# Optimization experiments

Measured on AMD Instinct MI355X. Metric: run time of the kernel, lower is better.

The kernel has to match this reference:

```python
import jax, jax.numpy as jnp
import numpy as np

B, S1, S2, H, DW = 64, 512, 512, 768, 200


def setup_inputs() -> dict:
    key = jax.random.key(0)
    ks = jax.random.split(key, 16)
    inp = {
        'x1': jax.random.normal(ks[0], (B, S1, H), jnp.float32),
        'x1_h': jax.random.normal(ks[1], (B, H), jnp.float32),
        'x1_mask': jax.random.randint(ks[2], (B, S1), 0, 2, jnp.int32),
        'y': jax.random.normal(ks[3], (B, S1), jnp.float32),
        'x2': jax.random.normal(ks[4], (B, S2, H), jnp.float32),
        'x2_h': jax.random.normal(ks[5], (B, H), jnp.float32),
        'x2_mask': jax.random.randint(ks[6], (B, S2), 0, 2, jnp.int32),
        'tt': jax.random.normal(ks[7], (B, S1, DW), jnp.float32),
        'tt2': jax.random.normal(ks[8], (B, S2, DW), jnp.float32),
        # parameters (xavier ~ N(0, 2/(fan_in+fan_out)))
        'W_bert': jax.random.normal(ks[9], (H + 1, H), jnp.float32) * np.sqrt(2.0 / (H + 1 + H)),
        'W_wv': jax.random.normal(ks[10], (DW + 1, DW), jnp.float32) * np.sqrt(2.0 / (DW + 1 + DW)),
        'lin_wv_w': jax.random.normal(ks[11], (DW, H), jnp.float32) * np.sqrt(1.0 / DW),
        'lin_wv_b': jnp.zeros((H,), jnp.float32),
        'lin_w': jax.random.normal(ks[12], (4 * H, 1), jnp.float32) * np.sqrt(1.0 / (4 * H)),
        'lin_b': jnp.zeros((1,), jnp.float32),
    }
    return inp


def _branch(x_cat, W, keys_vals, x1_inv, x2_inv):
    # x_cat: [B,S1,D+1], W: [D+1,D], keys_vals: [B,S2,D]
    xw = jnp.matmul(x_cat, W)                                  # [B,S1,D]
    a = jnp.einsum('bsd,btd->bst', xw, keys_vals)              # [B,S1,S2]
    a = jnp.where(x2_inv[:, None, :], jnp.float32(-1e-5), a)   # faithful: tiny mask value, pre-softmax
    a = jax.nn.softmax(a, axis=-1)
    v = jnp.einsum('bst,btd->bsd', a, keys_vals)               # [B,S1,D]
    v = jnp.where(x1_inv[:, :, None], jnp.float32(-1e5), v)
    return v.max(axis=1)                                       # max-pool over S1 -> [B,D]


def reference(x1, x1_h, x1_mask, y, x2, x2_h, x2_mask, tt, tt2,
              W_bert, W_wv, lin_wv_w, lin_wv_b, lin_w, lin_b):
    x1_inv = (1 - x1_mask).astype(bool)  # True where padded
    x2_inv = (1 - x2_mask).astype(bool)

    # word-vector branch
    x1_wv = jnp.concatenate([tt, y[:, :, None]], axis=-1)      # [B,S1,201]
    x12_wv = _branch(x1_wv, W_wv, tt2, x1_inv, x2_inv)         # [B,200]
    x12_wv = x12_wv @ lin_wv_w + lin_wv_b                      # [B,768]

    # bert branch
    x1c = jnp.concatenate([x1, y[:, :, None]], axis=-1)        # [B,S1,769]
    x12 = _branch(x1c, W_bert, x2, x1_inv, x2_inv)             # [B,768]

    h = jnp.concatenate([x1_h, x2_h, x12, x12_wv], axis=1)     # [B,3072]
    o = jax.nn.sigmoid(h @ lin_w + lin_b)                      # [B,1]
    return (o, x1_inv.astype(jnp.int32), x2_inv.astype(jnp.int32))
```

## Files before the change

### kernel.cpp

```cpp
#include <hip/hip_runtime.h>


#define BB 64
#define SS 512
#define HH 768
#define DWW 200

typedef __attribute__((ext_vector_type(8))) _Float16 f16x8;
typedef __attribute__((ext_vector_type(4))) _Float16 f16x4;
typedef __attribute__((ext_vector_type(4))) float f32x4;
typedef unsigned int u32;

__device__ __forceinline__ u32 fkey(float f) {
    u32 u = __float_as_uint(f);
    return (u & 0x80000000u) ? ~u : (u | 0x80000000u);
}
__device__ __forceinline__ float fdec(u32 k) {
    u32 u = (k & 0x80000000u) ? (k & 0x7fffffffu) : ~k;
    return __uint_as_float(u);
}
__device__ __forceinline__ f32x4 mm(f16x8 a, f16x8 b, f32x4 c) {
    return __builtin_amdgcn_mfma_f32_16x16x32_f16(a, b, c, 0, 0, 0);
}
__device__ __forceinline__ void gl16(const void* g, void* l) {
    __builtin_amdgcn_global_load_lds(
        (const __attribute__((address_space(1))) void*)g,
        (__attribute__((address_space(3))) void*)l, 16, 0, 0);
}

__global__ __launch_bounds__(256) void k_setup(
    const int* __restrict__ m1, const int* __restrict__ m2,
    const float* __restrict__ Wb, const float* __restrict__ Wwv,
    float* __restrict__ out, u32* __restrict__ k1, u32* __restrict__ k2,
    int* __restrict__ idx, int* __restrict__ rcnt,
    _Float16* __restrict__ wbTH, _Float16* __restrict__ wwTH) {
    int bid = blockIdx.x, tid = threadIdx.x;
    if (bid < 128) {
        int i = bid * 256 + tid;
        out[BB + i]           = (float)(1 - m1[i]);
        out[BB + BB * SS + i] = (float)(1 - m2[i]);
    } else if (bid < 320) {
        int i = (bid - 128) * 256 + tid;
        u32 v = fkey(-1e5f);
        if (i < BB * HH) k1[i] = v;
        if (i < BB * DWW) k2[i] = v;
    } else if (bid < 384) {
        int b = bid - 320;
        if (tid < 64) {
            int base = 0;
#pragma unroll
            for (int c = 0; c < 8; ++c) {
                int s = c * 64 + tid;
                int v = m1[b * SS + s];
                unsigned long long bal = __ballot(v != 0);
                int pre = __popcll(bal & ((1ull << tid) - 1ull));
                if (v) idx[b * SS + base + pre] = s;
                base += __popcll(bal);
            }
            if (tid == 0) rcnt[b] = base;
        }
    } else if (bid < 2784) {
        int i = (bid - 384) * 256 + tid;
        int n = i / 800, k = i - n * 800;
        wbTH[i] = (_Float16)((k < 769) ? Wb[(size_t)k * 768 + n] : 0.f);
    } else {
        int i = (bid - 2784) * 256 + tid;
        int n = i / 224, k = i - n * 224;
        wwTH[i] = (_Float16)((k < 201 && n < 200) ? Wwv[(size_t)k * 200 + n] : 0.f);
    }
}

__global__ __launch_bounds__(256) void k_prep(
    const float* __restrict__ x2, const float* __restrict__ tt2,
    const float* __restrict__ x1, const float* __restrict__ tt,
    const float* __restrict__ yv,
    const int* __restrict__ idx, const int* __restrict__ rcnt,
    _Float16* __restrict__ kvB, _Float16* __restrict__ kvTB,
    _Float16* __restrict__ kvW, _Float16* __restrict__ kvTW,
    _Float16* __restrict__ XcB, _Float16* __restrict__ XcW,
    int cb, int b0) {
    __shared__ float tile[64][65];
    int bx = blockIdx.x, tid = threadIdx.x;
    if (bx < cb * 128) {
        int cbi = bx >> 7, sub = bx & 127;
        int t0 = (sub & 7) * 64, ybr = sub >> 3;
        const float* src; _Float16* kv; _Float16* kvT; int D, DPAD, DTPAD, d0;
        if (ybr < 12) { src = x2;  kv = kvB; kvT = kvTB; D = 768; DPAD = 768; DTPAD = 768; d0 = ybr * 64; }
        else          { src = tt2; kv = kvW; kvT = kvTW; D = 200; DPAD = 256; DTPAD = 256; d0 = (ybr - 12) * 64; }
        int bg = b0 + cbi;
        int tq = tid >> 3, c8 = (tid & 7) * 8;
#pragma unroll
        for (int i = 0; i < 2; ++i) {
            int t = tq + i * 32;
            int gd = d0 + c8;
            float v[8];
            if (gd + 7 < D) {
                const float* rp = src + ((size_t)bg * SS + t0 + t) * D + gd;
                float4 p0 = *(const float4*)(rp);
                float4 p1 = *(const float4*)(rp + 4);
                v[0] = p0.x; v[1] = p0.y; v[2] = p0.z; v[3] = p0.w;
                v[4] = p1.x; v[5] = p1.y; v[6] = p1.z; v[7] = p1.w;
            } else {
#pragma unroll
                for (int j = 0; j < 8; ++j) {
                    int d = gd + j;
                    v[j] = (d < D) ? src[((size_t)bg * SS + t0 + t) * D + d] : 0.f;
                }
            }
            f16x8 o;
#pragma unroll
            for (int j = 0; j < 8; ++j) {
                tile[t][c8 + j] = v[j];
                o[j] = (_Float16)v[j];
            }
            *(f16x8*)(kv + ((size_t)cbi * SS + t0 + t) * DPAD + gd) = o;
        }
        __syncthreads();
#pragma unroll
        for (int i = 0; i < 2; ++i) {
            int dl = tq + i * 32, gdr = d0 + dl;
            f16x8 o;
#pragma unroll
            for (int j = 0; j < 8; ++j) o[j] = (_Float16)tile[c8 + j][dl];
            *(f16x8*)(kvT + ((size_t)cbi * DTPAD + gdr) * SS + t0 + c8) = o;
        }
    } else {
        bx -= cb * 128;
        int cbi = bx >> 8, xb = bx & 255;
        int bg = b0 + cbi;
        const float* X; _Float16* outp; int Din, KPAD; size_t ost;
        if (xb < 200) { X = x1; outp = XcB; Din = 768; KPAD = 800; ost = (size_t)cbi * 409600; }
        else { xb -= 200; X = tt; outp = XcW; Din = 200; KPAD = 224; ost = (size_t)cbi * 114688; }
        int i8 = (xb * 256 + tid) * 8;
        int s = i8 / KPAD, k0 = i8 - s * KPAD;
        int rc = rcnt[bg];
        int rpad = (rc + 127) & ~127;
        if (s >= rpad) return;
        f16x8 o = {};
        if (s < rc) {
            int sg = idx[bg * SS + s];
            const float* Xr = X + ((size_t)bg * SS + sg) * Din;
            if (k0 + 7 < Din) {
                float4 p0 = *(const float4*)(Xr + k0);
                float4 p1 = *(const float4*)(Xr + k0 + 4);
                o[0] = (_Float16)p0.x; o[1] = (_Float16)p0.y;
                o[2] = (_Float16)p0.z; o[3] = (_Float16)p0.w;
                o[4] = (_Float16)p1.x; o[5] = (_Float16)p1.y;
                o[6] = (_Float16)p1.z; o[7] = (_Float16)p1.w;
            } else {
#pragma unroll
                for (int j = 0; j < 8; ++j) {
                    int k = k0 + j;
                    float v = (k < Din) ? Xr[k]
                                        : ((k == Din) ? yv[(size_t)bg * SS + sg] : 0.f);
                    o[j] = (_Float16)v;
                }
            }
        }
        *(f16x8*)(outp + ost + (size_t)s * KPAD + k0) = o;
    }
}

template<int KA, int KST, int TN, int SXW, int DV, int AS, int BS, int EPI>
__device__ __forceinline__ void mm_core(
    const _Float16* __restrict__ A, const _Float16* __restrict__ B,
    _Float16* __restrict__ O, const float* __restrict__ rsum,
    u32* __restrict__ keys, int jb, const int* __restrict__ rcnt,
    int b0, char* lds, float* rsv) {
    int cbi = jb / (4 * TN);
    int rest = jb - cbi * (4 * TN);
    int ts = rest / TN, tn = rest - ts * TN;
    int s0 = ts * 128, n0 = tn * 128;

    int rc = rcnt[b0 + cbi];
    int rpad = (rc + 127) & ~127;
    if (s0 >= rpad) return;

    int tid = threadIdx.x, lane = tid & 63, wid = tid >> 6;
    int wr = wid >> 1, wc = wid & 1;
    int l15 = lane & 15, sl = lane >> 4, gb = sl * 4;

    const _Float16* srcA = A + (size_t)cbi * AS + (size_t)s0 * KA;
    const _Float16* srcB = B + (size_t)cbi * BS + (size_t)n0 * KA;

    if constexpr (EPI == 2) {
        if (tid < 128) rsv[tid] = rsum[cbi * SS + s0 + tid];
    }

    f32x4 zz = {0.f, 0.f, 0.f, 0.f};
    f32x4 acc[4][4];
#pragma unroll
    for (int i = 0; i < 4; ++i)
#pragma unroll
        for (int j = 0; j < 4; ++j) acc[i][j] = zz;

#define STAGE(buf, ks)                                                        \
    _Pragma("unroll") for (int i = 0; i < 4; ++i) {                           \
        int c = wid + 4 * i;                                                  \
        int arr = c >> 3, sub = c & 7, slot = sub >> 1, rh = sub & 1;         \
        const _Float16* gp = (arr ? srcB : srcA) +                            \
            (size_t)(rh * 64 + lane) * KA + (ks) * 32 + slot * 8;             \
        gl16(gp, lds + (buf) * 16384 + c * 1024);                             \
    }

    STAGE(0, 0);
    __syncthreads();
    int buf = 0;
#pragma unroll
    for (int ks = 0; ks < KST; ++ks) {
        if (ks + 1 < KST) STAGE(buf ^ 1, ks + 1);
        char* base = lds + buf * 16384;
        f16x8 a[4], b[4];
#pragma unroll
        for (int mf = 0; mf < 4; ++mf)
            a[mf] = *(const f16x8*)(base + sl * 2048 + (wr * 64 + mf * 16 + l15) * 16);
#pragma unroll
        for (int nf = 0; nf < 4; ++nf)
            b[nf] = *(const f16x8*)(base + 8192 + sl * 2048 + (wc * 64 + nf * 16 + l15) * 16);
#pragma unroll
        for (int mf = 0; mf < 4; ++mf)
#pragma unroll
            for (int nf = 0; nf < 4; ++nf)
                acc[mf][nf] = mm(a[mf], b[nf], acc[mf][nf]);
        __syncthreads();
        buf ^= 1;
    }
#undef STAGE

    if constexpr (EPI == 1) {
        _Float16* ce = (_Float16*)lds;
#pragma unroll
        for (int mf = 0; mf < 4; ++mf)
#pragma unroll
            for (int nf = 0; nf < 4; ++nf)
#pragma unroll
                for (int r = 0; r < 4; ++r) {
                    int row = wr * 64 + mf * 16 + gb + r;
                    int col = wc * 64 + nf * 16 + l15;
                    ce[row * 128 + col] = (_Float16)acc[mf][nf][r];
                }
        __syncthreads();
#pragma unroll
        for (int i = 0; i < 8; ++i) {
            int t = tid + i * 256;
            int row = t >> 4, col = (t & 15) * 8;
            *(f16x8*)(O + ((size_t)cbi * SS + s0 + row) * SXW + n0 + col) =
                *(const f16x8*)(ce + row * 128 + col);
        }
    } else {
        int bg = b0 + cbi;
#pragma unroll
        for (int nf = 0; nf < 4; ++nf) {
            float mx = -3.0e38f;
#pragma unroll
            for (int mf = 0; mf < 4; ++mf)
#pragma unroll
                for (int r = 0; r < 4; ++r) {
                    int srow = wr * 64 + mf * 16 + gb + r;
                    if (s0 + srow < rc) mx = fmaxf(mx, acc[mf][nf][r] * rsv[srow]);
                }
            mx = fmaxf(mx, __shfl_xor(mx, 16));
            mx = fmaxf(mx, __shfl_xor(mx, 32));
            if (lane < 16) {
                int d = n0 + wc * 64 + nf * 16 + lane;
                if (d < DV) atomicMax(&keys[(size_t)bg * DV + d], fkey(mx));
            }
        }
    }
}

template<int EPI,
         int KA0, int KST0, int TN0, int SXW0, int DV0, int AS0, int BS0,
         int KA1, int KST1, int TN1, int SXW1, int DV1, int AS1, int BS1>
__global__ __launch_bounds__(256) void k_mmM(
    const _Float16* __restrict__ A0, const _Float16* __restrict__ B0,
    _Float16* __restrict__ O0, const float* __restrict__ rs0, u32* __restrict__ key0,
    const _Float16* __restrict__ A1, const _Float16* __restrict__ B1,
    _Float16* __restrict__ O1, const float* __restrict__ rs1, u32* __restrict__ key1,
    int nj0, const int* __restrict__ rcnt, int b0, int nwg) {
    __shared__ __align__(16) char lds[32768];
    __shared__ float rsv[128];
    int bid = blockIdx.x;
    int x = bid & 7, t = bid >> 3;
    int tb = nj0 >> 3;
    int tw = (nwg - nj0) >> 3;
    if (t < tb)
        mm_core<KA0, KST0, TN0, SXW0, DV0, AS0, BS0, EPI>(
            A0, B0, O0, rs0, key0, x * tb + t, rcnt, b0, lds, rsv);
    else
        mm_core<KA1, KST1, TN1, SXW1, DV1, AS1, BS1, EPI>(
            A1, B1, O1, rs1, key1, x * tw + (t - tb), rcnt, b0, lds, rsv);
}

__global__ __launch_bounds__(256) void k_softmaxM(
    _Float16* __restrict__ SP0, float* __restrict__ rs0,
    _Float16* __restrict__ SP1, float* __restrict__ rs1,
    const int* __restrict__ m2, const int* __restrict__ rcnt, int nblk0, int b0) {
    int bid = blockIdx.x;
    bool selw = bid >= nblk0;
    int b = selw ? bid - nblk0 : bid;
    _Float16* SP = selw ? SP1 : SP0;
    float* rs = selw ? rs1 : rs0;
    int cbi = b >> 7, rb = b & 127;
    int wid = threadIdx.x >> 6, lane = threadIdx.x & 63;
    int row = rb * 4 + wid, bg = b0 + cbi;
    int rc = rcnt[bg];
    if (row >= rc) return;
    f16x8 sv = *(const f16x8*)(SP + ((size_t)cbi * SS + row) * SS + lane * 8);
    int4 q0 = *(const int4*)(m2 + bg * SS + lane * 8);
    int4 q1 = *(const int4*)(m2 + bg * SS + lane * 8 + 4);
    const int qm[8] = {q0.x, q0.y, q0.z, q0.w, q1.x, q1.y, q1.z, q1.w};
    float c[8];
#pragma unroll
    for (int j = 0; j < 8; ++j) c[j] = qm[j] ? (float)sv[j] : -1e-5f;
    float mx = c[0];
#pragma unroll
    for (int j = 1; j < 8; ++j) mx = fmaxf(mx, c[j]);
#pragma unroll
    for (int off = 1; off <= 32; off <<= 1) mx = fmaxf(mx, __shfl_xor(mx, off));
    f16x8 o;
    float sm = 0.f;
#pragma unroll
    for (int j = 0; j < 8; ++j) {
        _Float16 h = (_Float16)__expf(c[j] - mx);
        o[j] = h;
        sm += (float)h;
    }
#pragma unroll
    for (int off = 1; off <= 32; off <<= 1) sm += __shfl_xor(sm, off);
    *(f16x8*)(SP + ((size_t)cbi * SS + row) * SS + lane * 8) = o;
    if (lane == 0) rs[cbi * SS + row] = 1.0f / sm;
}

__global__ __launch_bounds__(256) void k_wvproj(const u32* __restrict__ wvkeys,
                                                const float* __restrict__ Wp,
                                                const float* __restrict__ bp,
                                                float* __restrict__ outp) {
    int b = blockIdx.x;
    __shared__ float xv[DWW];
    int tid = threadIdx.x;
    if (tid < DWW) xv[tid] = fdec(wvkeys[b * DWW + tid]);
    __syncthreads();
    for (int h = tid; h < HH; h += 256) {
        float acc = bp[h];
        for (int d = 0; d < DWW; ++d) acc += xv[d] * Wp[d * HH + h];
        outp[b * HH + h] = acc;
    }
}

__global__ __launch_bounds__(256) void k_final(const float* __restrict__ x1h,
                                               const float* __restrict__ x2h,
                                               const u32* __restrict__ keys,
                                               const float* __restrict__ wvp,
                                               const float* __restrict__ lw,
                                               const float* __restrict__ lb,
                                               float* __restrict__ out) {
    int b = blockIdx.x;
    int tid = threadIdx.x;
    float acc = 0.f;
    for (int i = tid; i < HH; i += 256) {
        acc += x1h[b * HH + i] * lw[i];
        acc += x2h[b * HH + i] * lw[HH + i];
        acc += fdec(keys[b * HH + i]) * lw[2 * HH + i];
        acc += wvp[b * HH + i] * lw[3 * HH + i];
    }
    __shared__ float red[4];
    int wid = tid >> 6, lane = tid & 63;
#pragma unroll
    for (int off = 32; off; off >>= 1) acc += __shfl_down(acc, off);
    if (lane == 0) red[wid] = acc;
    __syncthreads();
    if (tid == 0) {
        float z = red[0] + red[1] + red[2] + red[3] + lb[0];
        out[b] = 1.f / (1.f + __expf(-z));
    }
}

extern "C" void kernel_launch(void* const* d_in, const int* in_sizes, int n_in,
                              void* d_out, int out_size, void* d_ws, size_t ws_size,
                              hipStream_t stream) {
    const float* x1   = (const float*)d_in[0];
    const float* x1h  = (const float*)d_in[1];
    const int*   m1   = (const int*)d_in[2];
    const float* y    = (const float*)d_in[3];
    const float* x2   = (const float*)d_in[4];
    const float* x2h  = (const float*)d_in[5];
    const int*   m2   = (const int*)d_in[6];
    const float* tt   = (const float*)d_in[7];
    const float* tt2  = (const float*)d_in[8];
    const float* Wb   = (const float*)d_in[9];
    const float* Wwv  = (const float*)d_in[10];
    const float* lwvw = (const float*)d_in[11];
    const float* lwvb = (const float*)d_in[12];
    const float* lw   = (const float*)d_in[13];
    const float* lb   = (const float*)d_in[14];
    float* out = (float*)d_out;
    char* ws = (char*)d_ws;

    u32*      x12key   = (u32*)ws;
    u32*      x12wvkey = (u32*)(ws + 196608);
    float*    x12wvp   = (float*)(ws + 247808);
    float*    rsumB    = (float*)(ws + 444416);
    float*    rsumW    = (float*)(ws + 575488);
    _Float16* wbTH     = (_Float16*)(ws + 706560);
    _Float16* wwTH     = (_Float16*)(ws + 1935360);
    int*      idxBuf   = (int*)(ws + 2050048);
    int*      rcntBuf  = (int*)(ws + 2181120);
    const size_t D0 = 2181376;

    k_setup<<<3008, 256, 0, stream>>>(m1, m2, Wb, Wwv, out, x12key, x12wvkey,
                                      idxBuf, rcntBuf, wbTH, wwTH);

    const size_t perb = 4194304;
    int nb = 1;
    if (ws_size > D0 + perb) nb = (int)((ws_size - D0) / perb);
    if (nb > BB) nb = BB;
    if (nb < 1) nb = 1;

    char* R = ws + D0;
    _Float16* XcB = (_Float16*)R;
    _Float16* XcW = (_Float16*)(R + (size_t)nb * 819200);
    _Float16* S_b = (_Float16*)R;
    _Float16* S_w = (_Float16*)(R + (size_t)nb * 524288);
    char* p = R + (size_t)nb * 1048576;
    _Float16* XW_b = (_Float16*)p; p += (size_t)nb * 786432;
    _Float16* XW_w = (_Float16*)p; p += (size_t)nb * 262144;
    _Float16* KV_b = (_Float16*)p; p += (size_t)nb * 786432;
    _Float16* KV_w = (_Float16*)p; p += (size_t)nb * 262144;
    _Float16* KT_b = (_Float16*)p; p += (size_t)nb * 786432;
    _Float16* KT_w = (_Float16*)p;

    for (int b0 = 0; b0 < BB; b0 += nb) {
        int cb = (BB - b0 < nb) ? (BB - b0) : nb;
        k_prep<<<cb * 384, 256, 0, stream>>>(
            x2, tt2, x1, tt, y, idxBuf, rcntBuf,
            KV_b, KT_b, KV_w, KT_w, XcB, XcW, cb, b0);
        k_mmM<1, 800, 25, 6, 768, 0, 409600, 0,
                 224,  7, 2, 256, 0, 114688, 0><<<cb * 32, 256, 0, stream>>>(
            XcB, wbTH, XW_b, nullptr, nullptr,
            XcW, wwTH, XW_w, nullptr, nullptr,
            cb * 24, rcntBuf, b0, cb * 32);
        k_mmM<1, 768, 24, 4, 512, 0, 393216, 393216,
                 256,  8, 4, 512, 0, 131072, 131072><<<cb * 32, 256, 0, stream>>>(
            XW_b, KV_b, S_b, nullptr, nullptr,
            XW_w, KV_w, S_w, nullptr, nullptr,
            cb * 16, rcntBuf, b0, cb * 32);
        k_softmaxM<<<cb * 256, 256, 0, stream>>>(
            S_b, rsumB, S_w, rsumW, m2, rcntBuf, cb * 128, b0);
        k_mmM<2, 512, 16, 6, 0, 768, 262144, 393216,
                 512, 16, 2, 0, 200, 262144, 131072><<<cb * 32, 256, 0, stream>>>(
            S_b, KT_b, nullptr, rsumB, x12key,
            S_w, KT_w, nullptr, rsumW, x12wvkey,
            cb * 24, rcntBuf, b0, cb * 32);
    }

    k_wvproj<<<BB, 256, 0, stream>>>(x12wvkey, lwvw, lwvb, x12wvp);
    k_final<<<BB, 256, 0, stream>>>(x1h, x2h, x12key, x12wvp, lw, lb, out);
}
```

Baseline: 313.7 us.

## Fold setup work into prep kernel, widen KV transpose tiles, merge tail kernels

The big setup kernel is split up. Mask scanning moves to a small dedicated kernel, and the mask output, key init and weight transposes now ride as extra blocks in the first prep launch. The weight transposes also write four halves per thread. The KV transpose blocks now handle 128-wide d slabs with a larger LDS tile, which halves the number of KV blocks. The word-vector projection and final dot-product kernels merge into one tail kernel that keeps the projection in shared memory, removing a launch and a global round-trip. The risk is that the heavier per-block work and larger LDS use lower occupancy in prep.

```diff
diff --git a/kernel.cpp b/kernel.cpp
--- a/kernel.cpp
+++ b/kernel.cpp
@@ -28,71 +28,52 @@
         (__attribute__((address_space(3))) void*)l, 16, 0, 0);
 }
 
-__global__ __launch_bounds__(256) void k_setup(
-    const int* __restrict__ m1, const int* __restrict__ m2,
-    const float* __restrict__ Wb, const float* __restrict__ Wwv,
-    float* __restrict__ out, u32* __restrict__ k1, u32* __restrict__ k2,
-    int* __restrict__ idx, int* __restrict__ rcnt,
-    _Float16* __restrict__ wbTH, _Float16* __restrict__ wwTH) {
-    int bid = blockIdx.x, tid = threadIdx.x;
-    if (bid < 128) {
-        int i = bid * 256 + tid;
-        out[BB + i]           = (float)(1 - m1[i]);
-        out[BB + BB * SS + i] = (float)(1 - m2[i]);
-    } else if (bid < 320) {
-        int i = (bid - 128) * 256 + tid;
-        u32 v = fkey(-1e5f);
-        if (i < BB * HH) k1[i] = v;
-        if (i < BB * DWW) k2[i] = v;
-    } else if (bid < 384) {
-        int b = bid - 320;
-        if (tid < 64) {
-            int base = 0;
-#pragma unroll
-            for (int c = 0; c < 8; ++c) {
-                int s = c * 64 + tid;
-                int v = m1[b * SS + s];
-                unsigned long long bal = __ballot(v != 0);
-                int pre = __popcll(bal & ((1ull << tid) - 1ull));
-                if (v) idx[b * SS + base + pre] = s;
-                base += __popcll(bal);
-            }
-            if (tid == 0) rcnt[b] = base;
-        }
-    } else if (bid < 2784) {
-        int i = (bid - 384) * 256 + tid;
-        int n = i / 800, k = i - n * 800;
-        wbTH[i] = (_Float16)((k < 769) ? Wb[(size_t)k * 768 + n] : 0.f);
-    } else {
-        int i = (bid - 2784) * 256 + tid;
-        int n = i / 224, k = i - n * 224;
-        wwTH[i] = (_Float16)((k < 201 && n < 200) ? Wwv[(size_t)k * 200 + n] : 0.f);
-    }
+__global__ __launch_bounds__(64) void k_scan(const int* __restrict__ m1,
+                                             int* __restrict__ idx,
+                                             int* __restrict__ rcnt) {
+    int b = blockIdx.x, lane = threadIdx.x;
+    int base = 0;
+#pragma unroll
+    for (int c = 0; c < 8; ++c) {
+        int s = c * 64 + lane;
+        int v = m1[b * SS + s];
+        unsigned long long bal = __ballot(v != 0);
+        int pre = __popcll(bal & ((1ull << lane) - 1ull));
+        if (v) idx[b * SS + base + pre] = s;
+        base += __popcll(bal);
+    }
+    if (lane == 0) rcnt[b] = base;
 }
 
 __global__ __launch_bounds__(256) void k_prep(
     const float* __restrict__ x2, const float* __restrict__ tt2,
     const float* __restrict__ x1, const float* __restrict__ tt,
     const float* __restrict__ yv,
+    const int* __restrict__ m1, const int* __restrict__ m2,
+    const float* __restrict__ Wb, const float* __restrict__ Wwv,
     const int* __restrict__ idx, const int* __restrict__ rcnt,
     _Float16* __restrict__ kvB, _Float16* __restrict__ kvTB,
     _Float16* __restrict__ kvW, _Float16* __restrict__ kvTW,
     _Float16* __restrict__ XcB, _Float16* __restrict__ XcW,
+    float* __restrict__ out, u32* __restrict__ k1, u32* __restrict__ k2,
+    _Float16* __restrict__ wbTH, _Float16* __restrict__ wwTH,
     int cb, int b0) {
-    __shared__ float tile[64][65];
+    __shared__ float tile[64][132];
     int bx = blockIdx.x, tid = threadIdx.x;
-    if (bx < cb * 128) {
-        int cbi = bx >> 7, sub = bx & 127;
-        int t0 = (sub & 7) * 64, ybr = sub >> 3;
+    int NKV = cb * 64, NXC = cb * 256;
+
+    if (bx < NKV) {
+        int cbi = bx >> 6, sub = bx & 63;
+        int t0 = (sub & 7) * 64, slab = sub >> 3;
         const float* src; _Float16* kv; _Float16* kvT; int D, DPAD, DTPAD, d0;
-        if (ybr < 12) { src = x2;  kv = kvB; kvT = kvTB; D = 768; DPAD = 768; DTPAD = 768; d0 = ybr * 64; }
-        else          { src = tt2; kv = kvW; kvT = kvTW; D = 200; DPAD = 256; DTPAD = 256; d0 = (ybr - 12) * 64; }
+        if (slab < 6) { src = x2;  kv = kvB; kvT = kvTB; D = 768; DPAD = 768; DTPAD = 768; d0 = slab * 128; }
+        else          { src = tt2; kv = kvW; kvT = kvTW; D = 200; DPAD = 256; DTPAD = 256; d0 = (slab - 6) * 128; }
         int bg = b0 + cbi;
-        int tq = tid >> 3, c8 = (tid & 7) * 8;
-#pragma unroll
-        for (int i = 0; i < 2; ++i) {
-            int t = tq + i * 32;
-            int gd = d0 + c8;
+        int tr = tid >> 4, dc = (tid & 15) * 8;
+#pragma unroll
+        for (int i = 0; i < 4; ++i) {
+            int t = tr + i * 16;
+            int gd = d0 + dc;
             float v[8];
             if (gd + 7 < D) {
                 const float* rp = src + ((size_t)bg * SS + t0 + t) * D + gd;
@@ -110,23 +91,24 @@
             f16x8 o;
 #pragma unroll
             for (int j = 0; j < 8; ++j) {
-                tile[t][c8 + j] = v[j];
+                tile[t][dc + j] = v[j];
                 o[j] = (_Float16)v[j];
             }
             *(f16x8*)(kv + ((size_t)cbi * SS + t0 + t) * DPAD + gd) = o;
         }
         __syncthreads();
 #pragma unroll
-        for (int i = 0; i < 2; ++i) {
-            int dl = tq + i * 32, gdr = d0 + dl;
+        for (int i = 0; i < 4; ++i) {
+            int chunk = tid + i * 256;
+            int dl = chunk & 127, a = chunk >> 7;
             f16x8 o;
 #pragma unroll
-            for (int j = 0; j < 8; ++j) o[j] = (_Float16)tile[c8 + j][dl];
-            *(f16x8*)(kvT + ((size_t)cbi * DTPAD + gdr) * SS + t0 + c8) = o;
-        }
-    } else {
-        bx -= cb * 128;
-        int cbi = bx >> 8, xb = bx & 255;
+            for (int j = 0; j < 8; ++j) o[j] = (_Float16)tile[a * 8 + j][dl];
+            *(f16x8*)(kvT + ((size_t)cbi * DTPAD + d0 + dl) * SS + t0 + a * 8) = o;
+        }
+    } else if (bx < NKV + NXC) {
+        int u = bx - NKV;
+        int cbi = u >> 8, xb = u & 255;
         int bg = b0 + cbi;
         const float* X; _Float16* outp; int Din, KPAD; size_t ost;
         if (xb < 200) { X = x1; outp = XcB; Din = 768; KPAD = 800; ost = (size_t)cbi * 409600; }
@@ -158,6 +140,34 @@
             }
         }
         *(f16x8*)(outp + ost + (size_t)s * KPAD + k0) = o;
+    } else {
+        int u = bx - NKV - NXC;
+        if (u < 128) {
+            int i = u * 256 + tid;
+            out[BB + i]           = (float)(1 - m1[i]);
+            out[BB + BB * SS + i] = (float)(1 - m2[i]);
+        } else if (u < 320) {
+            int i = (u - 128) * 256 + tid;
+            u32 v = fkey(-1e5f);
+            if (i < BB * HH) k1[i] = v;
+            if (i < BB * DWW) k2[i] = v;
+        } else if (u < 920) {
+            int i = ((u - 320) * 256 + tid) * 4;
+            int n = i / 800, k = i - n * 800;
+            f16x4 o;
+#pragma unroll
+            for (int j = 0; j < 4; ++j)
+                o[j] = (_Float16)((k + j < 769) ? Wb[(size_t)(k + j) * 768 + n] : 0.f);
+            *(f16x4*)(wbTH + i) = o;
+        } else {
+            int i = ((u - 920) * 256 + tid) * 4;
+            int n = i / 224, k = i - n * 224;
+            f16x4 o;
+#pragma unroll
+            for (int j = 0; j < 4; ++j)
+                o[j] = (_Float16)((k + j < 201 && n < 200) ? Wwv[(size_t)(k + j) * 200 + n] : 0.f);
+            *(f16x4*)(wwTH + i) = o;
+        }
     }
 }
 
@@ -332,39 +342,31 @@
     if (lane == 0) rs[cbi * SS + row] = 1.0f / sm;
 }
 
-__global__ __launch_bounds__(256) void k_wvproj(const u32* __restrict__ wvkeys,
-                                                const float* __restrict__ Wp,
-                                                const float* __restrict__ bp,
-                                                float* __restrict__ outp) {
-    int b = blockIdx.x;
+__global__ __launch_bounds__(256) void k_tail(
+    const float* __restrict__ x1h, const float* __restrict__ x2h,
+    const u32* __restrict__ keys, const u32* __restrict__ wvkeys,
+    const float* __restrict__ Wp, const float* __restrict__ bp,
+    const float* __restrict__ lw, const float* __restrict__ lb,
+    float* __restrict__ out) {
+    int b = blockIdx.x, tid = threadIdx.x;
     __shared__ float xv[DWW];
-    int tid = threadIdx.x;
+    __shared__ float wvp[HH];
+    __shared__ float red[4];
     if (tid < DWW) xv[tid] = fdec(wvkeys[b * DWW + tid]);
     __syncthreads();
     for (int h = tid; h < HH; h += 256) {
         float acc = bp[h];
         for (int d = 0; d < DWW; ++d) acc += xv[d] * Wp[d * HH + h];
-        outp[b * HH + h] = acc;
-    }
-}
-
-__global__ __launch_bounds__(256) void k_final(const float* __restrict__ x1h,
-                                               const float* __restrict__ x2h,
-                                               const u32* __restrict__ keys,
-                                               const float* __restrict__ wvp,
-                                               const float* __restrict__ lw,
-                                               const float* __restrict__ lb,
-                                               float* __restrict__ out) {
-    int b = blockIdx.x;
-    int tid = threadIdx.x;
+        wvp[h] = acc;
+    }
+    __syncthreads();
     float acc = 0.f;
     for (int i = tid; i < HH; i += 256) {
         acc += x1h[b * HH + i] * lw[i];
         acc += x2h[b * HH + i] * lw[HH + i];
         acc += fdec(keys[b * HH + i]) * lw[2 * HH + i];
-        acc += wvp[b * HH + i] * lw[3 * HH + i];
-    }
-    __shared__ float red[4];
+        acc += wvp[i] * lw[3 * HH + i];
+    }
     int wid = tid >> 6, lane = tid & 63;
 #pragma unroll
     for (int off = 32; off; off >>= 1) acc += __shfl_down(acc, off);
@@ -399,7 +401,6 @@
 
     u32*      x12key   = (u32*)ws;
     u32*      x12wvkey = (u32*)(ws + 196608);
-    float*    x12wvp   = (float*)(ws + 247808);
     float*    rsumB    = (float*)(ws + 444416);
     float*    rsumW    = (float*)(ws + 575488);
     _Float16* wbTH     = (_Float16*)(ws + 706560);
@@ -407,9 +408,6 @@
     int*      idxBuf   = (int*)(ws + 2050048);
     int*      rcntBuf  = (int*)(ws + 2181120);
     const size_t D0 = 2181376;
-
-    k_setup<<<3008, 256, 0, stream>>>(m1, m2, Wb, Wwv, out, x12key, x12wvkey,
-                                      idxBuf, rcntBuf, wbTH, wwTH);
 
     const size_t perb = 4194304;
     int nb = 1;
@@ -430,11 +428,15 @@
     _Float16* KT_b = (_Float16*)p; p += (size_t)nb * 786432;
     _Float16* KT_w = (_Float16*)p;
 
+    k_scan<<<BB, 64, 0, stream>>>(m1, idxBuf, rcntBuf);
+
     for (int b0 = 0; b0 < BB; b0 += nb) {
         int cb = (BB - b0 < nb) ? (BB - b0) : nb;
-        k_prep<<<cb * 384, 256, 0, stream>>>(
-            x2, tt2, x1, tt, y, idxBuf, rcntBuf,
-            KV_b, KT_b, KV_w, KT_w, XcB, XcW, cb, b0);
+        int nprep = cb * 320 + ((b0 == 0) ? 976 : 0);
+        k_prep<<<nprep, 256, 0, stream>>>(
+            x2, tt2, x1, tt, y, m1, m2, Wb, Wwv, idxBuf, rcntBuf,
+            KV_b, KT_b, KV_w, KT_w, XcB, XcW,
+            out, x12key, x12wvkey, wbTH, wwTH, cb, b0);
         k_mmM<1, 800, 25, 6, 768, 0, 409600, 0,
                  224,  7, 2, 256, 0, 114688, 0><<<cb * 32, 256, 0, stream>>>(
             XcB, wbTH, XW_b, nullptr, nullptr,
@@ -454,6 +456,6 @@
             cb * 24, rcntBuf, b0, cb * 32);
     }
 
-    k_wvproj<<<BB, 256, 0, stream>>>(x12wvkey, lwvw, lwvb, x12wvp);
-    k_final<<<BB, 256, 0, stream>>>(x1h, x2h, x12key, x12wvp, lw, lb, out);
-}
+    k_tail<<<BB, 256, 0, stream>>>(x1h, x2h, x12key, x12wvkey,
+                                   lwvw, lwvb, lw, lb, out);
+}
```

Measured after the change: 326.5 us. 4.1% more time.
